# Optimization experiments

Hardware: AMD Instinct MI355X
Metric: run time of the kernel (lower is better)

Reference implementation:

```python
import jax, jax.numpy as jnp
import numpy as np

EMBED_DIM = 1024
NUM_HEADS = 16
HEAD_DIM = EMBED_DIM // NUM_HEADS
N, S = 4, 8192


def setup_inputs() -> dict:
    key = jax.random.key(0)
    ks = jax.random.split(key, 9)
    sc = 1.0 / np.sqrt(EMBED_DIM)
    d = {"x": jax.random.normal(ks[0], (N, S, EMBED_DIM), dtype=jnp.float32)}
    for i, name in enumerate(["Wq", "Wk", "Wv", "Wo"]):
        d[name] = jax.random.normal(ks[1 + i], (EMBED_DIM, EMBED_DIM), dtype=jnp.float32) * sc
    for i, name in enumerate(["bq", "bk", "bv", "bo"]):
        d[name] = jax.random.normal(ks[5 + i], (EMBED_DIM,), dtype=jnp.float32) * 0.01
    return d


def reference(x, Wq, Wk, Wv, Wo, bq, bk, bv, bo):
    n, s, e = x.shape
    # projections: nn.Linear => x @ W.T + b
    Q = x @ Wq.T + bq
    K = x @ Wk.T + bk
    V = x @ Wv.T + bv
    # (N, S, H, D) -> (N, H, S, D), matching torch .view().transpose(1, 2)
    Q = Q.reshape(n, s, NUM_HEADS, HEAD_DIM).transpose(0, 2, 1, 3)
    K = K.reshape(n, s, NUM_HEADS, HEAD_DIM).transpose(0, 2, 1, 3)
    V = V.reshape(n, s, NUM_HEADS, HEAD_DIM).transpose(0, 2, 1, 3)
    # Faithful to the original (buggy) einsum labeling: on (N,H,S,D) tensors
    # 'nqhd,nkhd->nhqk' attends OVER THE HEAD AXIS -> energy (N, S, H, H)
    energy = jnp.einsum('nqhd,nkhd->nhqk', Q, K)
    attention = jax.nn.softmax(energy / jnp.sqrt(jnp.float32(e)), axis=3)
    # out: (N, H, S, D), then reshaped as if (N, S, H*D) — exact original math
    out = jnp.einsum('nhql,nlhd->nqhd', attention, V).reshape(n, s, e)
    return out @ Wo.T + bo
```

## Files before the change

kernel.cpp:

```cpp
#include <hip/hip_runtime.h>
#include <cstdint>
#include <cstddef>

typedef unsigned short u16;
typedef __attribute__((ext_vector_type(8))) __bf16 bf16x8;
typedef __attribute__((ext_vector_type(4))) float floatx4;

typedef const __attribute__((address_space(1))) void* gptr_t;
typedef __attribute__((address_space(3))) void* lptr_t;

__device__ __forceinline__ u16 f2b(float f) {
    unsigned u = __builtin_bit_cast(unsigned, f);
    u += 0x7fffu + ((u >> 16) & 1u);
    return (u16)(u >> 16);
}

__global__ void cast_f32_bf16(const float* __restrict__ in, u16* __restrict__ out, int n4) {
    int i = blockIdx.x * blockDim.x + threadIdx.x;
    if (i < n4) {
        const float4 v = ((const float4*)in)[i];
        ushort4 o;
        o.x = f2b(v.x); o.y = f2b(v.y); o.z = f2b(v.z); o.w = f2b(v.w);
        ((ushort4*)out)[i] = o;
    }
}

template <bool OUT_BF16>
__global__ __launch_bounds__(256, 2)
void gemm_bt(const u16* __restrict__ A, const u16* __restrict__ B,
             const float* __restrict__ bias, void* __restrict__ Cout,
             int N, int K)
{
    __shared__ u16 lA[128 * 32];
    __shared__ u16 lB[128 * 32];

    const int tid  = threadIdx.x;
    const int m0   = blockIdx.y * 128;
    const int n0   = blockIdx.x * 128;
    const int row  = tid >> 2;
    const int chk  = tid & 3;
    const int lane = tid & 63;
    const int wv   = tid >> 6;
    const int wm   = wv >> 1;
    const int wn   = wv & 1;
    const int lrow = lane & 15;
    const int quad = lane >> 4;

    const u16* gA0 = A + (size_t)(m0 + row) * K + chk * 8;
    const u16* gB0 = B + (size_t)(n0 + row) * K + chk * 8;
    u16* sA0 = lA + tid * 8;
    u16* sB0 = lB + tid * 8;

    const u16* pA = lA + (wm * 64 + lrow) * 32 + quad * 8;
    const u16* pB = lB + (wn * 64 + lrow) * 32 + quad * 8;

    const floatx4 fzero = {0.f, 0.f, 0.f, 0.f};
    floatx4 acc[4][4];
    #pragma unroll
    for (int i = 0; i < 4; i++)
        #pragma unroll
        for (int j = 0; j < 4; j++) acc[i][j] = fzero;

    const size_t rstride = (size_t)64 * K;

    for (int k0 = 0; k0 < K; k0 += 32) {
        __builtin_amdgcn_global_load_lds((gptr_t)(gA0 + k0),           (lptr_t)sA0,          16, 0, 0);
        __builtin_amdgcn_global_load_lds((gptr_t)(gA0 + rstride + k0), (lptr_t)(sA0 + 2048), 16, 0, 0);
        __builtin_amdgcn_global_load_lds((gptr_t)(gB0 + k0),           (lptr_t)sB0,          16, 0, 0);
        __builtin_amdgcn_global_load_lds((gptr_t)(gB0 + rstride + k0), (lptr_t)(sB0 + 2048), 16, 0, 0);
        __syncthreads();

        bf16x8 af[4], bfr[4];
        #pragma unroll
        for (int i = 0; i < 4; i++) {
            af[i]  = *(const bf16x8*)(pA + i * 512);
            bfr[i] = *(const bf16x8*)(pB + i * 512);
        }
        #pragma unroll
        for (int i = 0; i < 4; i++)
            #pragma unroll
            for (int j = 0; j < 4; j++)
                acc[i][j] = __builtin_amdgcn_mfma_f32_16x16x32_bf16(af[i], bfr[j], acc[i][j], 0, 0, 0);
        __syncthreads();
    }

    float bsv[4];
    #pragma unroll
    for (int j = 0; j < 4; j++) bsv[j] = bias[n0 + wn * 64 + j * 16 + lrow];

    #pragma unroll
    for (int i = 0; i < 4; i++) {
        const int mbase = m0 + wm * 64 + i * 16 + quad * 4;
        #pragma unroll
        for (int j = 0; j < 4; j++) {
            const int n = n0 + wn * 64 + j * 16 + lrow;
            #pragma unroll
            for (int r = 0; r < 4; r++) {
                const float v = acc[i][j][r] + bsv[j];
                const size_t idx = (size_t)(mbase + r) * N + n;
                if constexpr (OUT_BF16) ((u16*)Cout)[idx] = f2b(v);
                else                    ((float*)Cout)[idx] = v;
            }
        }
    }
}

__global__ __launch_bounds__(256)
void attn(const u16* __restrict__ QKV, u16* __restrict__ Z)
{
    __shared__ __align__(16) u16 sV[4][1024];
    __shared__ __align__(16) u16 sA[4][640];
    __shared__ __align__(16) u16 sY[16 * 1152];

    const int tid  = threadIdx.x;
    const int lane = tid & 63;
    const int wv   = tid >> 6;
    const int lrow = lane & 15;
    const int quad = lane >> 4;
    const int pp   = lane >> 3;
    const int cc   = lane & 7;

    #pragma unroll
    for (int i = 0; i < 4; i++) {
        const int idx = i * 64 + lane;
        sA[wv][(idx >> 4) * 40 + 16 + (idx & 15)] = 0;
    }

    const int tgrp = blockIdx.x * 16;
    const int nb   = tgrp >> 13;
    const int sg   = (tgrp & 8191) >> 4;

    const floatx4 fzero = {0.f, 0.f, 0.f, 0.f};

    for (int tt = 0; tt < 4; tt++) {
        const int t = wv * 4 + tt;
        const u16* base = QKV + (size_t)(tgrp + t) * 3072;

        const bf16x8 q0 = *(const bf16x8*)(base + lrow * 64      + quad * 8);
        const bf16x8 q1 = *(const bf16x8*)(base + lrow * 64 + 32 + quad * 8);
        const bf16x8 k0 = *(const bf16x8*)(base + 1024 + lrow * 64      + quad * 8);
        const bf16x8 k1 = *(const bf16x8*)(base + 1024 + lrow * 64 + 32 + quad * 8);

        const u16* V = base + 2048;
        const bf16x8 va = *(const bf16x8*)(V + (2 * pp)     * 64 + cc * 8);
        const bf16x8 vb = *(const bf16x8*)(V + (2 * pp + 1) * 64 + cc * 8);
        #pragma unroll
        for (int s = 0; s < 8; s++) {
            const unsigned pv = (unsigned)__builtin_bit_cast(u16, (__bf16)va[s]) |
                                ((unsigned)__builtin_bit_cast(u16, (__bf16)vb[s]) << 16);
            *(unsigned*)&sV[wv][(s * 8 + cc) * 16 + 2 * pp] = pv;
        }

        floatx4 e = fzero;
        e = __builtin_amdgcn_mfma_f32_16x16x32_bf16(q0, k0, e, 0, 0, 0);
        e = __builtin_amdgcn_mfma_f32_16x16x32_bf16(q1, k1, e, 0, 0, 0);

        #pragma unroll
        for (int r = 0; r < 4; r++) {
            const float xv = e[r] * 0.03125f;
            float mx = xv;
            mx = fmaxf(mx, __shfl_xor(mx, 1));
            mx = fmaxf(mx, __shfl_xor(mx, 2));
            mx = fmaxf(mx, __shfl_xor(mx, 4));
            mx = fmaxf(mx, __shfl_xor(mx, 8));
            const float p = __expf(xv - mx);
            float s = p;
            s += __shfl_xor(s, 1);
            s += __shfl_xor(s, 2);
            s += __shfl_xor(s, 4);
            s += __shfl_xor(s, 8);
            sA[wv][(quad * 4 + r) * 40 + lrow] = f2b(p / s);
        }

        const bf16x8 af = *(const bf16x8*)&sA[wv][lrow * 40 + quad * 8];

        bf16x8 bfr[4];
        #pragma unroll
        for (int j = 0; j < 4; j++)
            #pragma unroll
            for (int jj = 0; jj < 8; jj++)
                bfr[j][jj] = __builtin_bit_cast(__bf16, (u16)0);
        if (quad < 2) {
            #pragma unroll
            for (int j = 0; j < 4; j++) {
                const int pr = (lrow & 7) * 8 + j * 2 + (lrow >> 3);
                bfr[j] = *(const bf16x8*)&sV[wv][pr * 16 + quad * 8];
            }
        }

        #pragma unroll
        for (int j = 0; j < 4; j++) {
            const floatx4 y = __builtin_amdgcn_mfma_f32_16x16x32_bf16(af, bfr[j], fzero, 0, 0, 0);
            #pragma unroll
            for (int r = 0; r < 4; r++)
                sY[t * 1152 + (quad * 4 + r) * 72 + j * 16 + lrow] = f2b(y[r]);
        }
    }

    __syncthreads();

    const int h   = tid >> 4;
    const int pos = tid & 15;
    u16* zrow = Z + (size_t)(nb * 8192 + h * 512 + sg) * 1024;
    #pragma unroll
    for (int it = 0; it < 8; it++) {
        const int c16 = it * 16 + pos;
        const int t = c16 >> 3, dc = c16 & 7;
        const uint4 v = *(const uint4*)&sY[t * 1152 + h * 72 + dc * 8];
        *(uint4*)(zrow + c16 * 8) = v;
    }
}

extern "C" void kernel_launch(void* const* d_in, const int* in_sizes, int n_in,
                              void* d_out, int out_size, void* d_ws, size_t ws_size,
                              hipStream_t stream)
{
    (void)in_sizes; (void)n_in; (void)out_size;
    const float* x  = (const float*)d_in[0];
    const float* Wq = (const float*)d_in[1];
    const float* Wk = (const float*)d_in[2];
    const float* Wv = (const float*)d_in[3];
    const float* Wo = (const float*)d_in[4];
    const float* bq = (const float*)d_in[5];
    const float* bk = (const float*)d_in[6];
    const float* bv = (const float*)d_in[7];
    const float* bo = (const float*)d_in[8];

    const size_t Mtot = 32768;
    char* ws = (char*)d_ws;
    u16*   Xbf  = (u16*)ws;
    u16*   Wqkv = (u16*)(ws + (64ull << 20));
    u16*   Wob  = (u16*)(ws + (64ull << 20) + (6ull << 20));
    float* bqkv = (float*)(ws + (72ull << 20));
    char*  dyn  = ws + (72ull << 20) + 16384;
    const size_t fixed = (72ull << 20) + 16384;

    int c = 4;
    for (int cc = 1; cc <= 4; cc <<= 1) {
        size_t Rr = Mtot / cc;
        if (fixed + Rr * 3072 * 2 + Rr * 1024 * 2 <= ws_size) { c = cc; break; }
    }
    const size_t R = Mtot / c;
    u16* QKV = (u16*)dyn;
    u16* Zb  = (u16*)(dyn + R * 3072 * 2);

    cast_f32_bf16<<<dim3(32768), dim3(256), 0, stream>>>(x, Xbf, (int)(Mtot * 1024 / 4));
    cast_f32_bf16<<<dim3(1024),  dim3(256), 0, stream>>>(Wq, Wqkv,           262144);
    cast_f32_bf16<<<dim3(1024),  dim3(256), 0, stream>>>(Wk, Wqkv + 1048576, 262144);
    cast_f32_bf16<<<dim3(1024),  dim3(256), 0, stream>>>(Wv, Wqkv + 2097152, 262144);
    cast_f32_bf16<<<dim3(1024),  dim3(256), 0, stream>>>(Wo, Wob,            262144);
    hipMemcpyAsync(bqkv,        bq, 1024 * sizeof(float), hipMemcpyDeviceToDevice, stream);
    hipMemcpyAsync(bqkv + 1024, bk, 1024 * sizeof(float), hipMemcpyDeviceToDevice, stream);
    hipMemcpyAsync(bqkv + 2048, bv, 1024 * sizeof(float), hipMemcpyDeviceToDevice, stream);

    for (int ci = 0; ci < c; ci++) {
        const u16* Ab   = Xbf + (size_t)ci * R * 1024;
        float*     outp = (float*)d_out + (size_t)ci * R * 1024;
        gemm_bt<true ><<<dim3(3072 / 128, (unsigned)(R / 128)), dim3(256), 0, stream>>>(Ab, Wqkv, bqkv, QKV, 3072, 1024);
        attn<<<dim3((unsigned)(R / 16)), dim3(256), 0, stream>>>(QKV, Zb);
        gemm_bt<false><<<dim3(1024 / 128, (unsigned)(R / 128)), dim3(256), 0, stream>>>(Zb, Wob, bo, outp, 1024, 1024);
    }
}
```

Before: 621.0 us.

## Merge cast launches, drop bias memcpys, use DPP reductions in softmax

Replaces four separate weight-cast launches with a single grid-stride kernel and removes the three bias device-to-device copies by selecting the bias pointer per column inside the QKV GEMM epilogue. The x cast now uses a grid-stride loop with fewer blocks. In the attention softmax, shuffle-xor reductions are replaced by DPP row_ror reductions and the division by a hardware reciprocal. The changes target launch overhead and softmax instruction cost, at the price of slightly lower reciprocal precision.

```diff
diff --git a/kernel.cpp b/kernel.cpp
--- a/kernel.cpp
+++ b/kernel.cpp
@@ -15,9 +15,20 @@
     return (u16)(u >> 16);
 }
 
-__global__ void cast_f32_bf16(const float* __restrict__ in, u16* __restrict__ out, int n4) {
-    int i = blockIdx.x * blockDim.x + threadIdx.x;
-    if (i < n4) {
+template <int N>
+__device__ __forceinline__ float ror_add(float x) {
+    int y = __builtin_amdgcn_update_dpp(0, __builtin_bit_cast(int, x), 0x120 + N, 0xF, 0xF, true);
+    return x + __builtin_bit_cast(float, y);
+}
+template <int N>
+__device__ __forceinline__ float ror_max(float x) {
+    int y = __builtin_amdgcn_update_dpp(0, __builtin_bit_cast(int, x), 0x120 + N, 0xF, 0xF, true);
+    return fmaxf(x, __builtin_bit_cast(float, y));
+}
+
+__global__ void cast_x(const float* __restrict__ in, u16* __restrict__ out, int n4) {
+    const int stride = gridDim.x * blockDim.x;
+    for (int i = blockIdx.x * blockDim.x + threadIdx.x; i < n4; i += stride) {
         const float4 v = ((const float4*)in)[i];
         ushort4 o;
         o.x = f2b(v.x); o.y = f2b(v.y); o.z = f2b(v.z); o.w = f2b(v.w);
@@ -25,11 +36,29 @@
     }
 }
 
+__global__ void cast_w(const float* __restrict__ Wq, const float* __restrict__ Wk,
+                       const float* __restrict__ Wv, const float* __restrict__ Wo,
+                       u16* __restrict__ Wqkv, u16* __restrict__ Wob) {
+    const int stride = gridDim.x * blockDim.x;
+    for (int i = blockIdx.x * blockDim.x + threadIdx.x; i < 1048576; i += stride) {
+        const int which = i >> 18;
+        const int local = i & 0x3FFFF;
+        const float* src = which == 0 ? Wq : which == 1 ? Wk : which == 2 ? Wv : Wo;
+        const float4 v = ((const float4*)src)[local];
+        ushort4 o;
+        o.x = f2b(v.x); o.y = f2b(v.y); o.z = f2b(v.z); o.w = f2b(v.w);
+        ushort4* dst = which < 3 ? (ushort4*)Wqkv + which * 262144 + local
+                                 : (ushort4*)Wob + local;
+        *dst = o;
+    }
+}
+
 template <bool OUT_BF16>
-__global__ __launch_bounds__(256, 2)
-void gemm_bt(const u16* __restrict__ A, const u16* __restrict__ B,
-             const float* __restrict__ bias, void* __restrict__ Cout,
-             int N, int K)
+__device__ __forceinline__
+void gemm_body(const u16* __restrict__ A, const u16* __restrict__ B,
+               const float* __restrict__ b0, const float* __restrict__ b1,
+               const float* __restrict__ b2, void* __restrict__ Cout,
+               int N, int K)
 {
     __shared__ u16 lA[128 * 32];
     __shared__ u16 lB[128 * 32];
@@ -86,7 +115,11 @@
 
     float bsv[4];
     #pragma unroll
-    for (int j = 0; j < 4; j++) bsv[j] = bias[n0 + wn * 64 + j * 16 + lrow];
+    for (int j = 0; j < 4; j++) {
+        const int n = n0 + wn * 64 + j * 16 + lrow;
+        const float* bp = n < 1024 ? b0 : (n < 2048 ? b1 : b2);
+        bsv[j] = bp[n & 1023];
+    }
 
     #pragma unroll
     for (int i = 0; i < 4; i++) {
@@ -105,8 +138,19 @@
     }
 }
 
+__global__ __launch_bounds__(256, 2)
+void gemm_qkv(const u16* __restrict__ A, const u16* __restrict__ B,
+              const float* __restrict__ b0, const float* __restrict__ b1,
+              const float* __restrict__ b2, u16* __restrict__ C, int N, int K)
+{ gemm_body<true>(A, B, b0, b1, b2, (void*)C, N, K); }
+
+__global__ __launch_bounds__(256, 2)
+void gemm_out(const u16* __restrict__ A, const u16* __restrict__ B,
+              const float* __restrict__ b0, float* __restrict__ C, int N, int K)
+{ gemm_body<false>(A, B, b0, b0, b0, (void*)C, N, K); }
+
 __global__ __launch_bounds__(256)
-void attn(const u16* __restrict__ QKV, u16* __restrict__ Z)
+void attn_v3(const u16* __restrict__ QKV, u16* __restrict__ Z)
 {
     __shared__ __align__(16) u16 sV[4][1024];
     __shared__ __align__(16) u16 sA[4][640];
@@ -159,17 +203,13 @@
         for (int r = 0; r < 4; r++) {
             const float xv = e[r] * 0.03125f;
             float mx = xv;
-            mx = fmaxf(mx, __shfl_xor(mx, 1));
-            mx = fmaxf(mx, __shfl_xor(mx, 2));
-            mx = fmaxf(mx, __shfl_xor(mx, 4));
-            mx = fmaxf(mx, __shfl_xor(mx, 8));
+            mx = ror_max<1>(mx); mx = ror_max<2>(mx);
+            mx = ror_max<4>(mx); mx = ror_max<8>(mx);
             const float p = __expf(xv - mx);
             float s = p;
-            s += __shfl_xor(s, 1);
-            s += __shfl_xor(s, 2);
-            s += __shfl_xor(s, 4);
-            s += __shfl_xor(s, 8);
-            sA[wv][(quad * 4 + r) * 40 + lrow] = f2b(p / s);
+            s = ror_add<1>(s); s = ror_add<2>(s);
+            s = ror_add<4>(s); s = ror_add<8>(s);
+            sA[wv][(quad * 4 + r) * 40 + lrow] = f2b(p * __builtin_amdgcn_rcpf(s));
         }
 
         const bf16x8 af = *(const bf16x8*)&sA[wv][lrow * 40 + quad * 8];
@@ -228,12 +268,11 @@
 
     const size_t Mtot = 32768;
     char* ws = (char*)d_ws;
-    u16*   Xbf  = (u16*)ws;
-    u16*   Wqkv = (u16*)(ws + (64ull << 20));
-    u16*   Wob  = (u16*)(ws + (64ull << 20) + (6ull << 20));
-    float* bqkv = (float*)(ws + (72ull << 20));
-    char*  dyn  = ws + (72ull << 20) + 16384;
-    const size_t fixed = (72ull << 20) + 16384;
+    u16* Xbf  = (u16*)ws;
+    u16* Wqkv = (u16*)(ws + (64ull << 20));
+    u16* Wob  = (u16*)(ws + (64ull << 20) + (6ull << 20));
+    char* dyn = ws + (72ull << 20);
+    const size_t fixed = (72ull << 20);
 
     int c = 4;
     for (int cc = 1; cc <= 4; cc <<= 1) {
@@ -244,20 +283,14 @@
     u16* QKV = (u16*)dyn;
     u16* Zb  = (u16*)(dyn + R * 3072 * 2);
 
-    cast_f32_bf16<<<dim3(32768), dim3(256), 0, stream>>>(x, Xbf, (int)(Mtot * 1024 / 4));
-    cast_f32_bf16<<<dim3(1024),  dim3(256), 0, stream>>>(Wq, Wqkv,           262144);
-    cast_f32_bf16<<<dim3(1024),  dim3(256), 0, stream>>>(Wk, Wqkv + 1048576, 262144);
-    cast_f32_bf16<<<dim3(1024),  dim3(256), 0, stream>>>(Wv, Wqkv + 2097152, 262144);
-    cast_f32_bf16<<<dim3(1024),  dim3(256), 0, stream>>>(Wo, Wob,            262144);
-    hipMemcpyAsync(bqkv,        bq, 1024 * sizeof(float), hipMemcpyDeviceToDevice, stream);
-    hipMemcpyAsync(bqkv + 1024, bk, 1024 * sizeof(float), hipMemcpyDeviceToDevice, stream);
-    hipMemcpyAsync(bqkv + 2048, bv, 1024 * sizeof(float), hipMemcpyDeviceToDevice, stream);
+    cast_x<<<dim3(4096), dim3(256), 0, stream>>>(x, Xbf, (int)(Mtot * 1024 / 4));
+    cast_w<<<dim3(1024), dim3(256), 0, stream>>>(Wq, Wk, Wv, Wo, Wqkv, Wob);
 
     for (int ci = 0; ci < c; ci++) {
         const u16* Ab   = Xbf + (size_t)ci * R * 1024;
         float*     outp = (float*)d_out + (size_t)ci * R * 1024;
-        gemm_bt<true ><<<dim3(3072 / 128, (unsigned)(R / 128)), dim3(256), 0, stream>>>(Ab, Wqkv, bqkv, QKV, 3072, 1024);
-        attn<<<dim3((unsigned)(R / 16)), dim3(256), 0, stream>>>(QKV, Zb);
-        gemm_bt<false><<<dim3(1024 / 128, (unsigned)(R / 128)), dim3(256), 0, stream>>>(Zb, Wob, bo, outp, 1024, 1024);
-    }
-}
+        gemm_qkv<<<dim3(24, (unsigned)(R / 128)), dim3(256), 0, stream>>>(Ab, Wqkv, bq, bk, bv, QKV, 3072, 1024);
+        attn_v3<<<dim3((unsigned)(R / 16)), dim3(256), 0, stream>>>(QKV, Zb);
+        gemm_out<<<dim3(8, (unsigned)(R / 128)), dim3(256), 0, stream>>>(Zb, Wob, bo, outp, 1024, 1024);
+    }
+}
```

Result: no change. 615.0 us (-1.0%).
